# Kernel tuning notes

Hardware: AMD Instinct MI355X
Metric: run time of the kernel (lower is better)

Reference implementation:

```python
import jax, jax.numpy as jnp
from jax import lax
import numpy as np


def setup_inputs() -> dict:
    key = jax.random.key(0)
    im = jax.random.normal(key, (16, 3, 1024, 1024), dtype=jnp.float32)
    return {"im": im, "levels": 4}


def _pyr_reduce(x, kern):
    # replicate-pad by 2 on each spatial side (matches the torch.cat edge copies)
    xp = jnp.pad(x, ((0, 0), (0, 0), (2, 2), (2, 2)), mode="edge")
    # original: valid 5x5 conv then [0::2, 0::2] slice == stride-2 valid conv
    # depthwise over the 3 channels (same kernel each channel)
    return lax.conv_general_dilated(
        xp, kern,
        window_strides=(2, 2), padding="VALID",
        dimension_numbers=("NCHW", "OIHW", "NCHW"),
        feature_group_count=3,
    )


def reference(im, levels):
    kvec = jnp.array([0.0625, 0.25, 0.375, 0.25, 0.0625], dtype=im.dtype)
    k2 = jnp.outer(kvec, kvec)                       # kernel1 = kernelv * kernelh
    kern = jnp.broadcast_to(k2, (3, 1, 5, 5))        # depthwise OIHW
    gpyr = [im]
    for _ in range(levels - 1):
        gpyr.append(_pyr_reduce(gpyr[-1], kern))
    return tuple(gpyr)
```

## Files before the change

### kernel.cpp

```cpp
#include <hip/hip_runtime.h>


struct Row { float4 A, B, C, D; };

template <int WIN>
__device__ __forceinline__ Row loadrow(const float* ip, int iy, int xb) {
    const float4* p = (const float4*)(ip + (size_t)iy * WIN + xb);
    Row r; r.A = p[0]; r.B = p[1]; r.C = p[2]; r.D = p[3];
    return r;
}

__device__ __forceinline__ void remap(Row& w, bool l, bool r) {
    const float4 A = w.A, B = w.B, C = w.C, D = w.D;
    w.A.z = l ? A.x : (r ? B.z : A.z);
    w.A.w = l ? A.x : (r ? B.w : A.w);
    w.B.x = l ? A.x : (r ? C.x : B.x);
    w.B.y = l ? A.y : (r ? C.y : B.y);
    w.B.z = l ? A.z : (r ? C.z : B.z);
    w.B.w = l ? A.w : (r ? C.w : B.w);
    w.C.x = l ? B.x : (r ? D.x : C.x);
    w.C.y = l ? B.y : (r ? D.y : C.y);
    w.C.z = l ? B.z : (r ? D.z : C.z);
    w.C.w = l ? B.w : (r ? D.w : C.w);
    w.D.x = l ? C.x : (r ? D.w : D.x);
}

__device__ __forceinline__ float4 hconv(const Row& w) {
    const float k0 = 0.0625f, k1 = 0.25f, k2 = 0.375f;
    float4 h;
    h.x = k0 * (w.A.z + w.B.z) + k1 * (w.A.w + w.B.y) + k2 * w.B.x;
    h.y = k0 * (w.B.x + w.C.x) + k1 * (w.B.y + w.B.w) + k2 * w.B.z;
    h.z = k0 * (w.B.z + w.C.z) + k1 * (w.B.w + w.C.y) + k2 * w.C.x;
    h.w = k0 * (w.C.x + w.D.x) + k1 * (w.C.y + w.C.w) + k2 * w.C.z;
    return h;
}

template <int R, int HIN, int WIN, bool FUSE>
__global__ __launch_bounds__(256) void gpyr_slide(
        const float* __restrict__ in,
        float* __restrict__ out0,
        float* __restrict__ out1) {
    constexpr int HOUT = HIN / 2, WOUT = WIN / 2;
    const int tx = threadIdx.x, ty = threadIdx.y;
    const int ox0 = (blockIdx.x * blockDim.x + tx) * 4;
    const int Y0  = (blockIdx.y * blockDim.y + ty) * R;
    const int img = blockIdx.z;

    const bool left  = (ox0 == 0);
    const bool right = (2 * ox0 + 12 > WIN);
    int xb = 2 * ox0 - 4;
    if (left)  xb = 0;
    if (right) xb = WIN - 16;

    const float* ip = in + (size_t)img * HIN * WIN;
    float* o1 = out1 + (size_t)img * HOUT * WOUT;
    float* o0 = out0 + (size_t)img * HIN * WIN;

    Row r0 = loadrow<WIN>(ip, max(2 * Y0 - 2, 0), xb);
    Row r1 = loadrow<WIN>(ip, max(2 * Y0 - 1, 0), xb);
    Row r2 = loadrow<WIN>(ip, 2 * Y0, xb);
    Row ra = loadrow<WIN>(ip, 2 * Y0 + 1, xb);
    Row rb = loadrow<WIN>(ip, min(2 * Y0 + 2, HIN - 1), xb);

    remap(r0, left, right); remap(r1, left, right); remap(r2, left, right);
    float4 hs0 = hconv(r0), hs1 = hconv(r1), hs2 = hconv(r2);
    float4 qlo = r2.B, qhi = r2.C;

    const float k0 = 0.0625f, k1 = 0.25f, k2 = 0.375f;

#pragma unroll
    for (int i = 0; i < R; ++i) {
        const int oy = Y0 + i;

        Row ran, rbn;
        if (i + 1 < R) {
            ran = loadrow<WIN>(ip, 2 * (oy + 1) + 1, xb);
            rbn = loadrow<WIN>(ip, min(2 * (oy + 1) + 2, HIN - 1), xb);
        }

        remap(ra, left, right);
        remap(rb, left, right);

        if (FUSE) {
            float* op = o0 + (size_t)(2 * oy) * WIN + 2 * ox0;
            *(float4*)(op)     = qlo;
            *(float4*)(op + 4) = qhi;
            float* op1 = o0 + (size_t)(2 * oy + 1) * WIN + 2 * ox0;
            *(float4*)(op1)     = ra.B;
            *(float4*)(op1 + 4) = ra.C;
        }

        float4 ha = hconv(ra), hb = hconv(rb);
        qlo = rb.B; qhi = rb.C;

        float4 o;
        o.x = k0 * (hs0.x + hb.x) + k1 * (hs1.x + ha.x) + k2 * hs2.x;
        o.y = k0 * (hs0.y + hb.y) + k1 * (hs1.y + ha.y) + k2 * hs2.y;
        o.z = k0 * (hs0.z + hb.z) + k1 * (hs1.z + ha.z) + k2 * hs2.z;
        o.w = k0 * (hs0.w + hb.w) + k1 * (hs1.w + ha.w) + k2 * hs2.w;
        *(float4*)(o1 + (size_t)oy * WOUT + ox0) = o;

        hs0 = hs2; hs1 = ha; hs2 = hb;
        ra = ran; rb = rbn;
    }
}

extern "C" void kernel_launch(void* const* d_in, const int* in_sizes, int n_in,
                              void* d_out, int out_size, void* d_ws, size_t ws_size,
                              hipStream_t stream) {
    const float* im = (const float*)d_in[0];
    float* out = (float*)d_out;

    const int NC = 16 * 3;
    const size_t L0 = (size_t)NC * 1024 * 1024;
    const size_t L1 = (size_t)NC * 512 * 512;
    const size_t L2 = (size_t)NC * 256 * 256;

    float* out0 = out;
    float* out1 = out0 + L0;
    float* out2 = out1 + L1;
    float* out3 = out2 + L2;

    {
        dim3 block(64, 4, 1);
        dim3 grid(2, 512 / (4 * 8), NC);
        gpyr_slide<8, 1024, 1024, true><<<grid, block, 0, stream>>>(im, out0, out1);
    }
    {
        dim3 block(64, 4, 1);
        dim3 grid(1, 256 / (4 * 4), NC);
        gpyr_slide<4, 512, 512, false><<<grid, block, 0, stream>>>(out1, nullptr, out2);
    }
    {
        dim3 block(32, 8, 1);
        dim3 grid(1, 128 / (8 * 2), NC);
        gpyr_slide<2, 256, 256, false><<<grid, block, 0, stream>>>(out2, nullptr, out3);
    }
}
```

Measured before the change: 126.4 us.

## Halve per-thread output width to double thread count in pyramid kernels

Each thread now produces 2 output pixels per row instead of 4, while still loading a 16-float window. This doubles the grid in x and gives the third level a 64x4 block. The edge remapping is rewritten as an extract step with separate left and two right-edge cases, and the fused copy of level 0 now writes one float4 per row per thread. The aim is more parallelism and latency hiding, at the cost of extra redundant input loads, since neighbouring threads' windows overlap more.

```diff
diff --git a/kernel.cpp b/kernel.cpp
--- a/kernel.cpp
+++ b/kernel.cpp
@@ -1,37 +1,35 @@
 #include <hip/hip_runtime.h>
 
 
-struct Row { float4 A, B, C, D; };
+struct Row4 { float4 A, B, C, D; };
 
 template <int WIN>
-__device__ __forceinline__ Row loadrow(const float* ip, int iy, int xb) {
+__device__ __forceinline__ Row4 load4(const float* ip, int iy, int xb) {
     const float4* p = (const float4*)(ip + (size_t)iy * WIN + xb);
-    Row r; r.A = p[0]; r.B = p[1]; r.C = p[2]; r.D = p[3];
+    Row4 r; r.A = p[0]; r.B = p[1]; r.C = p[2]; r.D = p[3];
     return r;
 }
 
-__device__ __forceinline__ void remap(Row& w, bool l, bool r) {
-    const float4 A = w.A, B = w.B, C = w.C, D = w.D;
-    w.A.z = l ? A.x : (r ? B.z : A.z);
-    w.A.w = l ? A.x : (r ? B.w : A.w);
-    w.B.x = l ? A.x : (r ? C.x : B.x);
-    w.B.y = l ? A.y : (r ? C.y : B.y);
-    w.B.z = l ? A.z : (r ? C.z : B.z);
-    w.B.w = l ? A.w : (r ? C.w : B.w);
-    w.C.x = l ? B.x : (r ? D.x : C.x);
-    w.C.y = l ? B.y : (r ? D.y : C.y);
-    w.C.z = l ? B.z : (r ? D.z : C.z);
-    w.C.w = l ? B.w : (r ? D.w : C.w);
-    w.D.x = l ? C.x : (r ? D.w : D.x);
+__device__ __forceinline__ void extract(const Row4& r, bool L, bool R1, bool R2,
+                                        float w[7], float4& cp) {
+    w[0] = L ? r.A.x : R1 ? r.B.z : R2 ? r.C.z : r.A.z;
+    w[1] = L ? r.A.x : R1 ? r.B.w : R2 ? r.C.w : r.A.w;
+    w[2] = L ? r.A.x : R1 ? r.C.x : R2 ? r.D.x : r.B.x;
+    w[3] = L ? r.A.y : R1 ? r.C.y : R2 ? r.D.y : r.B.y;
+    w[4] = L ? r.A.z : R1 ? r.C.z : R2 ? r.D.z : r.B.z;
+    w[5] = L ? r.A.w : R1 ? r.C.w : R2 ? r.D.w : r.B.w;
+    w[6] = L ? r.B.x : R1 ? r.D.x : R2 ? r.D.w : r.C.x;
+    cp.x = L ? r.A.x : R1 ? r.C.x : R2 ? r.D.x : r.B.x;
+    cp.y = L ? r.A.y : R1 ? r.C.y : R2 ? r.D.y : r.B.y;
+    cp.z = L ? r.A.z : R1 ? r.C.z : R2 ? r.D.z : r.B.z;
+    cp.w = L ? r.A.w : R1 ? r.C.w : R2 ? r.D.w : r.B.w;
 }
 
-__device__ __forceinline__ float4 hconv(const Row& w) {
+__device__ __forceinline__ float2 hconv2(const float w[7]) {
     const float k0 = 0.0625f, k1 = 0.25f, k2 = 0.375f;
-    float4 h;
-    h.x = k0 * (w.A.z + w.B.z) + k1 * (w.A.w + w.B.y) + k2 * w.B.x;
-    h.y = k0 * (w.B.x + w.C.x) + k1 * (w.B.y + w.B.w) + k2 * w.B.z;
-    h.z = k0 * (w.B.z + w.C.z) + k1 * (w.B.w + w.C.y) + k2 * w.C.x;
-    h.w = k0 * (w.C.x + w.D.x) + k1 * (w.C.y + w.C.w) + k2 * w.C.z;
+    float2 h;
+    h.x = k0 * (w[0] + w[4]) + k1 * (w[1] + w[3]) + k2 * w[2];
+    h.y = k0 * (w[2] + w[6]) + k1 * (w[3] + w[5]) + k2 * w[4];
     return h;
 }
 
@@ -42,29 +40,36 @@
         float* __restrict__ out1) {
     constexpr int HOUT = HIN / 2, WOUT = WIN / 2;
     const int tx = threadIdx.x, ty = threadIdx.y;
-    const int ox0 = (blockIdx.x * blockDim.x + tx) * 4;
+    const int g   = blockIdx.x * 64 + tx;
     const int Y0  = (blockIdx.y * blockDim.y + ty) * R;
     const int img = blockIdx.z;
 
-    const bool left  = (ox0 == 0);
-    const bool right = (2 * ox0 + 12 > WIN);
-    int xb = 2 * ox0 - 4;
-    if (left)  xb = 0;
-    if (right) xb = WIN - 16;
+    const int x4 = 4 * g;
+    const bool L  = (g == 0);
+    const bool R1 = (x4 == WIN - 8);
+    const bool R2 = (x4 == WIN - 4);
+    int xb = x4 - 4;
+    if (L) xb = 0;
+    if (R1 || R2) xb = WIN - 16;
 
     const float* ip = in + (size_t)img * HIN * WIN;
     float* o1 = out1 + (size_t)img * HOUT * WOUT;
     float* o0 = out0 + (size_t)img * HIN * WIN;
 
-    Row r0 = loadrow<WIN>(ip, max(2 * Y0 - 2, 0), xb);
-    Row r1 = loadrow<WIN>(ip, max(2 * Y0 - 1, 0), xb);
-    Row r2 = loadrow<WIN>(ip, 2 * Y0, xb);
-    Row ra = loadrow<WIN>(ip, 2 * Y0 + 1, xb);
-    Row rb = loadrow<WIN>(ip, min(2 * Y0 + 2, HIN - 1), xb);
+    float2 hs0, hs1, hs2;
+    float4 cpE;
+    {
+        Row4 t0 = load4<WIN>(ip, max(2 * Y0 - 2, 0), xb);
+        Row4 t1 = load4<WIN>(ip, max(2 * Y0 - 1, 0), xb);
+        Row4 t2 = load4<WIN>(ip, 2 * Y0, xb);
+        float w[7]; float4 cp;
+        extract(t0, L, R1, R2, w, cp); hs0 = hconv2(w);
+        extract(t1, L, R1, R2, w, cp); hs1 = hconv2(w);
+        extract(t2, L, R1, R2, w, cpE); hs2 = hconv2(w);
+    }
 
-    remap(r0, left, right); remap(r1, left, right); remap(r2, left, right);
-    float4 hs0 = hconv(r0), hs1 = hconv(r1), hs2 = hconv(r2);
-    float4 qlo = r2.B, qhi = r2.C;
+    Row4 ra = load4<WIN>(ip, 2 * Y0 + 1, xb);
+    Row4 rb = load4<WIN>(ip, min(2 * Y0 + 2, HIN - 1), xb);
 
     const float k0 = 0.0625f, k1 = 0.25f, k2 = 0.375f;
 
@@ -72,33 +77,32 @@
     for (int i = 0; i < R; ++i) {
         const int oy = Y0 + i;
 
-        Row ran, rbn;
+        Row4 ran, rbn;
         if (i + 1 < R) {
-            ran = loadrow<WIN>(ip, 2 * (oy + 1) + 1, xb);
-            rbn = loadrow<WIN>(ip, min(2 * (oy + 1) + 2, HIN - 1), xb);
+            ran = load4<WIN>(ip, 2 * oy + 3, xb);
+            rbn = load4<WIN>(ip, min(2 * oy + 4, HIN - 1), xb);
         }
 
-        remap(ra, left, right);
-        remap(rb, left, right);
-
         if (FUSE) {
-            float* op = o0 + (size_t)(2 * oy) * WIN + 2 * ox0;
-            *(float4*)(op)     = qlo;
-            *(float4*)(op + 4) = qhi;
-            float* op1 = o0 + (size_t)(2 * oy + 1) * WIN + 2 * ox0;
-            *(float4*)(op1)     = ra.B;
-            *(float4*)(op1 + 4) = ra.C;
+            *(float4*)(o0 + (size_t)(2 * oy) * WIN + x4) = cpE;
         }
 
-        float4 ha = hconv(ra), hb = hconv(rb);
-        qlo = rb.B; qhi = rb.C;
+        float wa[7]; float4 cpA;
+        extract(ra, L, R1, R2, wa, cpA);
+        if (FUSE) {
+            *(float4*)(o0 + (size_t)(2 * oy + 1) * WIN + x4) = cpA;
+        }
+        float2 ha = hconv2(wa);
 
-        float4 o;
+        float wb[7]; float4 cpB;
+        extract(rb, L, R1, R2, wb, cpB);
+        float2 hb = hconv2(wb);
+        cpE = cpB;
+
+        float2 o;
         o.x = k0 * (hs0.x + hb.x) + k1 * (hs1.x + ha.x) + k2 * hs2.x;
         o.y = k0 * (hs0.y + hb.y) + k1 * (hs1.y + ha.y) + k2 * hs2.y;
-        o.z = k0 * (hs0.z + hb.z) + k1 * (hs1.z + ha.z) + k2 * hs2.z;
-        o.w = k0 * (hs0.w + hb.w) + k1 * (hs1.w + ha.w) + k2 * hs2.w;
-        *(float4*)(o1 + (size_t)oy * WOUT + ox0) = o;
+        *(float2*)(o1 + (size_t)oy * WOUT + 2 * g) = o;
 
         hs0 = hs2; hs1 = ha; hs2 = hb;
         ra = ran; rb = rbn;
@@ -123,17 +127,17 @@
 
     {
         dim3 block(64, 4, 1);
-        dim3 grid(2, 512 / (4 * 8), NC);
+        dim3 grid(4, 512 / (4 * 8), NC);
         gpyr_slide<8, 1024, 1024, true><<<grid, block, 0, stream>>>(im, out0, out1);
     }
     {
         dim3 block(64, 4, 1);
-        dim3 grid(1, 256 / (4 * 4), NC);
+        dim3 grid(2, 256 / (4 * 4), NC);
         gpyr_slide<4, 512, 512, false><<<grid, block, 0, stream>>>(out1, nullptr, out2);
     }
     {
-        dim3 block(32, 8, 1);
-        dim3 grid(1, 128 / (8 * 2), NC);
+        dim3 block(64, 4, 1);
+        dim3 grid(1, 128 / (4 * 2), NC);
         gpyr_slide<2, 256, 256, false><<<grid, block, 0, stream>>>(out2, nullptr, out3);
     }
 }
```

Measured after the change: 321.4 us. +154.3%, slower.
